# Performance work log

Measured on AMD Instinct MI355X. Metric: run time of the kernel, lower is better.

Reference implementation:

```python
import jax, jax.numpy as jnp
import numpy as np
from math import sqrt

DIM = 64
N_HEADS = 12
B, T = 4, 2048


def setup_inputs() -> dict:
    key = jax.random.key(0)
    ks = jax.random.split(key, 5)
    scale = 1.0 / sqrt(DIM)
    x = jax.random.normal(ks[0], (B, T, DIM), dtype=jnp.float32)
    # torch Linear(dim, h*dim) weight is (h*dim, dim); store transposed (dim, h*dim)
    Wq = jax.random.uniform(ks[1], (DIM, N_HEADS * DIM), dtype=jnp.float32, minval=-scale, maxval=scale)
    Wk = jax.random.uniform(ks[2], (DIM, N_HEADS * DIM), dtype=jnp.float32, minval=-scale, maxval=scale)
    Wv = jax.random.uniform(ks[3], (DIM, N_HEADS * DIM), dtype=jnp.float32, minval=-scale, maxval=scale)
    # finalDense: Linear(h*dim, dim) -> stored (h*dim, dim)
    Wo = jax.random.uniform(ks[4], (N_HEADS * DIM, DIM), dtype=jnp.float32,
                            minval=-1.0 / sqrt(N_HEADS * DIM), maxval=1.0 / sqrt(N_HEADS * DIM))
    return {"x": x, "Wq": Wq, "Wk": Wk, "Wv": Wv, "Wo": Wo}


def reference(x, Wq, Wk, Wv, Wo):
    b, t, k = x.shape
    h = Wq.shape[1] // k
    # NOTE: the original module does .view(b,t,h,k).view(b*h,t,k), a flat
    # row-major memory reinterpretation (NOT a head transpose). jnp.reshape
    # is the same flat reshape, so this is faithful.
    Q = (x @ Wq).reshape(b * h, t, k)
    K = (x @ Wk).reshape(b * h, t, k)
    V = (x @ Wv).reshape(b * h, t, k)
    # W[b,i,j] = sum_k K[b,i,k] * Q[b,j,k], scaled; softmax over j (last dim)
    W = jnp.einsum('bik,bjk->bij', K, Q) / sqrt(k)
    W = jax.nn.softmax(W, axis=2)
    Z = jnp.einsum('bij,bjk->bik', W, V)  # (b*h, t, k)
    Z = Z.reshape(b, t, h * k)  # flat reinterpretation, matches torch views
    return Z @ Wo
```

## Files before the change

kernel.cpp:

```cpp
#include <hip/hip_runtime.h>
#include <hip/hip_bf16.h>


#define DIM 64
#define NH 12
#define HD 768
#define BT 8192
#define TSEQ 2048
#define NSLICE 48
#define SLICE (TSEQ*DIM)

#define LDQ 72
#define LDP 72
#define LDT 72

typedef unsigned short ushort;
typedef __attribute__((ext_vector_type(8))) short bf16x8;
typedef __attribute__((ext_vector_type(4))) float f32x4;

#define SCALE2 0.18033688011112042f

__device__ __forceinline__ ushort f2b(float f) {
    union { float f; unsigned int i; } v; v.f = f;
    unsigned int x = v.i;
    return (ushort)((x + 0x7fffu + ((x >> 16) & 1u)) >> 16);
}

__global__ __launch_bounds__(256) void prep_w(
    const float* __restrict__ Wq, const float* __restrict__ Wk,
    const float* __restrict__ Wv, const float* __restrict__ Wo,
    ushort* __restrict__ Wt, ushort* __restrict__ Wot)
{
    __shared__ float tile[64][65];
    int bx = blockIdx.x;
    int z = bx / 12, bt = bx % 12;
    const float* __restrict__ IN = (z == 0) ? Wq : (z == 1) ? Wk : (z == 2) ? Wv : Wo;
    int inStride  = (z < 3) ? HD : DIM;
    int outStride = (z < 3) ? DIM : HD;
    int rbase = (z < 3) ? 0 : bt * 64;
    int cbase = (z < 3) ? bt * 64 : 0;
    ushort* __restrict__ OUT = (z < 3) ? (Wt + (size_t)z * HD * DIM) : Wot;
    int t = threadIdx.x;
    int r = t >> 2, c0 = (t & 3) * 16;
    #pragma unroll
    for (int cc = 0; cc < 16; cc += 4) {
        float4 a = *(const float4*)&IN[(size_t)(rbase + r) * inStride + cbase + c0 + cc];
        tile[r][c0 + cc] = a.x; tile[r][c0 + cc + 1] = a.y;
        tile[r][c0 + cc + 2] = a.z; tile[r][c0 + cc + 3] = a.w;
    }
    __syncthreads();
    int cl = t >> 2, r0 = (t & 3) * 16;
    ushort tmp[16] __attribute__((aligned(16)));
    #pragma unroll
    for (int rr = 0; rr < 16; ++rr) tmp[rr] = f2b(tile[r0 + rr][cl]);
    *(float4*)&OUT[(size_t)(cbase + cl) * outStride + rbase + r0] = *(const float4*)tmp;
    *(float4*)&OUT[(size_t)(cbase + cl) * outStride + rbase + r0 + 8] = *(const float4*)&tmp[8];
}

__global__ __launch_bounds__(256) void qkv_kernel(
    const float* __restrict__ x, const ushort* __restrict__ Wt,
    ushort* __restrict__ Q, ushort* __restrict__ K, ushort* __restrict__ V)
{
    int rt = blockIdx.x, half = blockIdx.y;
    int t = threadIdx.x, w = t >> 6, lane = t & 63;
    int ln = lane & 15, q = lane >> 4;
    int m0 = rt * 64 + w * 16;

    float4 xa = *(const float4*)&x[(size_t)(m0 + ln) * DIM + q * 8];
    float4 xb_ = *(const float4*)&x[(size_t)(m0 + ln) * DIM + q * 8 + 4];
    float4 xc = *(const float4*)&x[(size_t)(m0 + ln) * DIM + 32 + q * 8];
    float4 xd = *(const float4*)&x[(size_t)(m0 + ln) * DIM + 32 + q * 8 + 4];
    ushort ta[8] __attribute__((aligned(16)));
    ushort tb[8] __attribute__((aligned(16)));
    ta[0]=f2b(xa.x); ta[1]=f2b(xa.y); ta[2]=f2b(xa.z); ta[3]=f2b(xa.w);
    ta[4]=f2b(xb_.x); ta[5]=f2b(xb_.y); ta[6]=f2b(xb_.z); ta[7]=f2b(xb_.w);
    tb[0]=f2b(xc.x); tb[1]=f2b(xc.y); tb[2]=f2b(xc.z); tb[3]=f2b(xc.w);
    tb[4]=f2b(xd.x); tb[5]=f2b(xd.y); tb[6]=f2b(xd.z); tb[7]=f2b(xd.w);
    bf16x8 af0 = *(const bf16x8*)ta;
    bf16x8 af1 = *(const bf16x8*)tb;

    for (int cc = 0; cc < 18; ++cc) {
        int ct = half * 18 + cc;
        int which = ct / 12;
        int col0 = (ct % 12) * 64;
        const ushort* __restrict__ Wz = Wt + (size_t)which * HD * DIM;
        ushort* __restrict__ Y = (which == 0) ? Q : (which == 1) ? K : V;
        float sc = (which == 0) ? SCALE2 : 1.f;
        #pragma unroll
        for (int nt = 0; nt < 4; ++nt) {
            int n = col0 + nt * 16 + ln;
            bf16x8 bf0 = *(const bf16x8*)&Wz[(size_t)n * DIM + q * 8];
            bf16x8 bf1 = *(const bf16x8*)&Wz[(size_t)n * DIM + 32 + q * 8];
            f32x4 acc = (f32x4){0.f, 0.f, 0.f, 0.f};
            acc = __builtin_amdgcn_mfma_f32_16x16x32_bf16(af0, bf0, acc, 0, 0, 0);
            acc = __builtin_amdgcn_mfma_f32_16x16x32_bf16(af1, bf1, acc, 0, 0, 0);
            #pragma unroll
            for (int r = 0; r < 4; ++r)
                Y[(size_t)(m0 + q * 4 + r) * HD + col0 + nt * 16 + ln] = f2b(acc[r] * sc);
        }
    }
}

__global__ __launch_bounds__(256) void vtrans_kernel(
    const ushort* __restrict__ V, ushort* __restrict__ Vt)
{
    __shared__ ushort tileT[64 * LDT];
    int tt = blockIdx.x, s = blockIdx.y;
    const ushort* __restrict__ Vp = V + (size_t)s * SLICE;
    ushort* __restrict__ Vo = Vt + (size_t)s * SLICE;
    int t = threadIdx.x;
    int r = t >> 3, c = (t & 7) * 8;
    ushort va[8] __attribute__((aligned(16)));
    ushort vb[8] __attribute__((aligned(16)));
    *(float4*)va = *(const float4*)&Vp[(size_t)(tt * 64 + r) * DIM + c];
    *(float4*)vb = *(const float4*)&Vp[(size_t)(tt * 64 + r + 32) * DIM + c];
    int g0 = ((r >> 3) ^ (c >> 3)) * 8 + (r & 7);
    int g1 = (((r + 32) >> 3) ^ (c >> 3)) * 8 + (r & 7);
    #pragma unroll
    for (int k = 0; k < 8; ++k) {
        tileT[(c + k) * LDT + g0] = va[k];
        tileT[(c + k) * LDT + g1] = vb[k];
    }
    __syncthreads();
    #pragma unroll
    for (int j = 0; j < 2; ++j) {
        int flat = t + 256 * j;
        int d = flat >> 3, tg = flat & 7;
        int sg = tg ^ ((d >> 3) & 7);
        float4 vv = *(const float4*)&tileT[d * LDT + sg * 8];
        *(float4*)&Vo[(size_t)d * TSEQ + tt * 64 + tg * 8] = vv;
    }
}

__global__ __launch_bounds__(256) void attn_kernel(
    const ushort* __restrict__ Qs, const ushort* __restrict__ Ks,
    const ushort* __restrict__ Vts, ushort* __restrict__ Zs)
{
    __shared__ ushort Qt[64 * LDQ];
    __shared__ ushort Pw[128 * LDP];
    int itile = blockIdx.x, s = blockIdx.y;
    const ushort* __restrict__ Qp = Qs + (size_t)s * SLICE;
    const ushort* __restrict__ Kp = Ks + (size_t)s * SLICE;
    const ushort* __restrict__ Vp = Vts + (size_t)s * SLICE;
    ushort* __restrict__ Zp = Zs + (size_t)s * SLICE;
    int t = threadIdx.x, w = t >> 6, lane = t & 63;
    int ln = lane & 15, q = lane >> 4;

    bf16x8 kf[2][2];
    #pragma unroll
    for (int ih = 0; ih < 2; ++ih) {
        int i0 = itile * 128 + w * 32 + ih * 16 + ln;
        kf[ih][0] = *(const bf16x8*)&Kp[(size_t)i0 * DIM + q * 8];
        kf[ih][1] = *(const bf16x8*)&Kp[(size_t)i0 * DIM + 32 + q * 8];
    }
    f32x4 Of[2][4];
    #pragma unroll
    for (int ih = 0; ih < 2; ++ih)
        #pragma unroll
        for (int dt = 0; dt < 4; ++dt) Of[ih][dt] = (f32x4){0.f, 0.f, 0.f, 0.f};
    float lsum[2] = {0.f, 0.f};
    ushort* Pme = &Pw[w * 32 * LDP];

    int sr = t >> 3, sc = (t & 7) * 8;
    float4 qa0 = *(const float4*)&Qp[(size_t)sr * DIM + sc];
    float4 qa1 = *(const float4*)&Qp[(size_t)(sr + 32) * DIM + sc];

    for (int jt = 0; jt < TSEQ; jt += 64) {
        __syncthreads();
        *(float4*)&Qt[sr * LDQ + sc] = qa0;
        *(float4*)&Qt[(sr + 32) * LDQ + sc] = qa1;
        __syncthreads();
        if (jt + 64 < TSEQ) {
            qa0 = *(const float4*)&Qp[(size_t)(jt + 64 + sr) * DIM + sc];
            qa1 = *(const float4*)&Qp[(size_t)(jt + 64 + sr + 32) * DIM + sc];
        }
        bf16x8 vb[4][2];
        #pragma unroll
        for (int dt = 0; dt < 4; ++dt) {
            vb[dt][0] = *(const bf16x8*)&Vp[(size_t)(dt * 16 + ln) * TSEQ + jt + q * 8];
            vb[dt][1] = *(const bf16x8*)&Vp[(size_t)(dt * 16 + ln) * TSEQ + jt + 32 + q * 8];
        }

        f32x4 Sf[2][4];
        #pragma unroll
        for (int mt = 0; mt < 4; ++mt) {
            bf16x8 a0 = *(const bf16x8*)&Qt[(mt * 16 + ln) * LDQ + q * 8];
            bf16x8 a1 = *(const bf16x8*)&Qt[(mt * 16 + ln) * LDQ + 32 + q * 8];
            #pragma unroll
            for (int ih = 0; ih < 2; ++ih) {
                f32x4 acc = (f32x4){0.f, 0.f, 0.f, 0.f};
                acc = __builtin_amdgcn_mfma_f32_16x16x32_bf16(a0, kf[ih][0], acc, 0, 0, 0);
                acc = __builtin_amdgcn_mfma_f32_16x16x32_bf16(a1, kf[ih][1], acc, 0, 0, 0);
                Sf[ih][mt] = acc;
            }
        }
        #pragma unroll
        for (int ih = 0; ih < 2; ++ih) {
            float ls = 0.f;
            #pragma unroll
            for (int mt = 0; mt < 4; ++mt) {
                float p0 = __builtin_amdgcn_exp2f(Sf[ih][mt][0]);
                float p1 = __builtin_amdgcn_exp2f(Sf[ih][mt][1]);
                float p2 = __builtin_amdgcn_exp2f(Sf[ih][mt][2]);
                float p3 = __builtin_amdgcn_exp2f(Sf[ih][mt][3]);
                unsigned int b0 = __float_as_uint(p0), b1 = __float_as_uint(p1);
                unsigned int b2 = __float_as_uint(p2), b3 = __float_as_uint(p3);
                unsigned int t1 = b1 & 0xFFFF0000u, t3 = b3 & 0xFFFF0000u;
                unsigned int h01 = (b0 >> 16) | t1;
                unsigned int h23 = (b2 >> 16) | t3;
                ls += __uint_as_float(h01 << 16) + __uint_as_float(t1)
                    + __uint_as_float(h23 << 16) + __uint_as_float(t3);
                *(uint2*)&Pme[(ih * 16 + ln) * LDP + mt * 16 + q * 4] =
                    make_uint2(h01, h23);
            }
            lsum[ih] += ls;
        }
        bf16x8 pa[2][2];
        #pragma unroll
        for (int ih = 0; ih < 2; ++ih) {
            pa[ih][0] = *(const bf16x8*)&Pme[(ih * 16 + ln) * LDP + q * 8];
            pa[ih][1] = *(const bf16x8*)&Pme[(ih * 16 + ln) * LDP + 32 + q * 8];
        }
        #pragma unroll
        for (int dt = 0; dt < 4; ++dt)
            #pragma unroll
            for (int ih = 0; ih < 2; ++ih) {
                Of[ih][dt] = __builtin_amdgcn_mfma_f32_16x16x32_bf16(pa[ih][0], vb[dt][0], Of[ih][dt], 0, 0, 0);
                Of[ih][dt] = __builtin_amdgcn_mfma_f32_16x16x32_bf16(pa[ih][1], vb[dt][1], Of[ih][dt], 0, 0, 0);
            }
    }
    float linv_r[2][4];
    #pragma unroll
    for (int ih = 0; ih < 2; ++ih) {
        float l = lsum[ih];
        l += __shfl_xor(l, 16);
        l += __shfl_xor(l, 32);
        float linv = 1.f / l;
        #pragma unroll
        for (int r = 0; r < 4; ++r) linv_r[ih][r] = __shfl(linv, q * 4 + r);
    }
    #pragma unroll
    for (int ih = 0; ih < 2; ++ih)
        #pragma unroll
        for (int dt = 0; dt < 4; ++dt)
            #pragma unroll
            for (int r = 0; r < 4; ++r)
                Pme[(ih * 16 + q * 4 + r) * LDP + dt * 16 + ln] =
                    f2b(Of[ih][dt][r] * linv_r[ih][r]);
    __syncthreads();
    int zr = t >> 1, zc = (t & 1) * 32;
    size_t zoff = (size_t)(itile * 128 + zr) * DIM + zc;
    #pragma unroll
    for (int c4 = 0; c4 < 4; ++c4)
        *(float4*)&Zp[zoff + c4 * 8] = *(const float4*)&Pw[zr * LDP + zc + c4 * 8];
}

__global__ __launch_bounds__(64) void out_kernel(
    const ushort* __restrict__ Z, const ushort* __restrict__ Wot,
    float* __restrict__ out)
{
    int m0 = blockIdx.x * 16;
    int lane = threadIdx.x;
    int ln = lane & 15, q = lane >> 4;
    f32x4 acc[4];
    #pragma unroll
    for (int nt = 0; nt < 4; ++nt) acc[nt] = (f32x4){0.f, 0.f, 0.f, 0.f};
    for (int kc = 0; kc < 24; ++kc) {
        bf16x8 af = *(const bf16x8*)&Z[(size_t)(m0 + ln) * HD + kc * 32 + q * 8];
        #pragma unroll
        for (int nt = 0; nt < 4; ++nt) {
            bf16x8 bf = *(const bf16x8*)&Wot[(size_t)(nt * 16 + ln) * HD + kc * 32 + q * 8];
            acc[nt] = __builtin_amdgcn_mfma_f32_16x16x32_bf16(af, bf, acc[nt], 0, 0, 0);
        }
    }
    #pragma unroll
    for (int nt = 0; nt < 4; ++nt)
        #pragma unroll
        for (int r = 0; r < 4; ++r)
            out[(size_t)(m0 + q * 4 + r) * DIM + nt * 16 + ln] = acc[nt][r];
}

extern "C" void kernel_launch(void* const* d_in, const int* in_sizes, int n_in,
                              void* d_out, int out_size, void* d_ws, size_t ws_size,
                              hipStream_t stream)
{
    const float* x  = (const float*)d_in[0];
    const float* Wq = (const float*)d_in[1];
    const float* Wk = (const float*)d_in[2];
    const float* Wv = (const float*)d_in[3];
    const float* Wo = (const float*)d_in[4];
    float* out = (float*)d_out;

    const size_t n = (size_t)BT * HD;
    ushort* Q   = (ushort*)d_ws;
    ushort* K   = Q + n;
    ushort* V   = K + n;
    ushort* Vt  = V + n;
    ushort* Wt  = Vt;
    ushort* Wot = Vt + n;
    ushort* Z   = V;

    prep_w<<<48, 256, 0, stream>>>(Wq, Wk, Wv, Wo, Wt, Wot);
    qkv_kernel<<<dim3(128, 2), 256, 0, stream>>>(x, Wt, Q, K, V);
    vtrans_kernel<<<dim3(32, 48), 256, 0, stream>>>(V, Vt);
    attn_kernel<<<dim3(16, 48), 256, 0, stream>>>(Q, K, Vt, Z);
    out_kernel<<<512, 64, 0, stream>>>(Z, Wot, out);
}
```

Baseline: 208.8 us.

## Use two waves of 64 rows each and stage V tiles through LDS

The attention kernel now runs 128 threads per block instead of 256, and each wave handles 64 query rows instead of 32. This halves the number of waves that reload the shared Q/V tile and doubles the MFMA work per LDS fragment. V is prefetched into registers with coalesced loads and staged in a shared Vtile, replacing the per-wave strided global loads of V fragments. In exchange each wave holds more accumulator registers (Of and Sf double), which may lower occupancy, and each block has fewer waves to hide latency.

```diff
diff --git a/kernel.cpp b/kernel.cpp
--- a/kernel.cpp
+++ b/kernel.cpp
@@ -132,11 +132,12 @@
     }
 }
 
-__global__ __launch_bounds__(256) void attn_kernel(
+__global__ __launch_bounds__(128) void attn_kernel(
     const ushort* __restrict__ Qs, const ushort* __restrict__ Ks,
     const ushort* __restrict__ Vts, ushort* __restrict__ Zs)
 {
     __shared__ ushort Qt[64 * LDQ];
+    __shared__ ushort Vtile[64 * LDQ];
     __shared__ ushort Pw[128 * LDP];
     int itile = blockIdx.x, s = blockIdx.y;
     const ushort* __restrict__ Qp = Qs + (size_t)s * SLICE;
@@ -146,48 +147,52 @@
     int t = threadIdx.x, w = t >> 6, lane = t & 63;
     int ln = lane & 15, q = lane >> 4;
 
-    bf16x8 kf[2][2];
-    #pragma unroll
-    for (int ih = 0; ih < 2; ++ih) {
-        int i0 = itile * 128 + w * 32 + ih * 16 + ln;
+    bf16x8 kf[4][2];
+    #pragma unroll
+    for (int ih = 0; ih < 4; ++ih) {
+        int i0 = itile * 128 + w * 64 + ih * 16 + ln;
         kf[ih][0] = *(const bf16x8*)&Kp[(size_t)i0 * DIM + q * 8];
         kf[ih][1] = *(const bf16x8*)&Kp[(size_t)i0 * DIM + 32 + q * 8];
     }
-    f32x4 Of[2][4];
-    #pragma unroll
-    for (int ih = 0; ih < 2; ++ih)
+    f32x4 Of[4][4];
+    #pragma unroll
+    for (int ih = 0; ih < 4; ++ih)
         #pragma unroll
         for (int dt = 0; dt < 4; ++dt) Of[ih][dt] = (f32x4){0.f, 0.f, 0.f, 0.f};
-    float lsum[2] = {0.f, 0.f};
-    ushort* Pme = &Pw[w * 32 * LDP];
+    float lsum[4] = {0.f, 0.f, 0.f, 0.f};
+    ushort* Pme = &Pw[w * 64 * LDP];
 
     int sr = t >> 3, sc = (t & 7) * 8;
-    float4 qa0 = *(const float4*)&Qp[(size_t)sr * DIM + sc];
-    float4 qa1 = *(const float4*)&Qp[(size_t)(sr + 32) * DIM + sc];
+    float4 qa[4], va[4];
+    #pragma unroll
+    for (int k = 0; k < 4; ++k) {
+        qa[k] = *(const float4*)&Qp[(size_t)(sr + 16 * k) * DIM + sc];
+        va[k] = *(const float4*)&Vp[(size_t)(sr + 16 * k) * TSEQ + sc];
+    }
 
     for (int jt = 0; jt < TSEQ; jt += 64) {
         __syncthreads();
-        *(float4*)&Qt[sr * LDQ + sc] = qa0;
-        *(float4*)&Qt[(sr + 32) * LDQ + sc] = qa1;
+        #pragma unroll
+        for (int k = 0; k < 4; ++k) {
+            *(float4*)&Qt[(sr + 16 * k) * LDQ + sc] = qa[k];
+            *(float4*)&Vtile[(sr + 16 * k) * LDQ + sc] = va[k];
+        }
         __syncthreads();
         if (jt + 64 < TSEQ) {
-            qa0 = *(const float4*)&Qp[(size_t)(jt + 64 + sr) * DIM + sc];
-            qa1 = *(const float4*)&Qp[(size_t)(jt + 64 + sr + 32) * DIM + sc];
-        }
-        bf16x8 vb[4][2];
-        #pragma unroll
-        for (int dt = 0; dt < 4; ++dt) {
-            vb[dt][0] = *(const bf16x8*)&Vp[(size_t)(dt * 16 + ln) * TSEQ + jt + q * 8];
-            vb[dt][1] = *(const bf16x8*)&Vp[(size_t)(dt * 16 + ln) * TSEQ + jt + 32 + q * 8];
-        }
-
-        f32x4 Sf[2][4];
+            #pragma unroll
+            for (int k = 0; k < 4; ++k) {
+                qa[k] = *(const float4*)&Qp[(size_t)(jt + 64 + sr + 16 * k) * DIM + sc];
+                va[k] = *(const float4*)&Vp[(size_t)(sr + 16 * k) * TSEQ + jt + 64 + sc];
+            }
+        }
+
+        f32x4 Sf[4][4];
         #pragma unroll
         for (int mt = 0; mt < 4; ++mt) {
             bf16x8 a0 = *(const bf16x8*)&Qt[(mt * 16 + ln) * LDQ + q * 8];
             bf16x8 a1 = *(const bf16x8*)&Qt[(mt * 16 + ln) * LDQ + 32 + q * 8];
             #pragma unroll
-            for (int ih = 0; ih < 2; ++ih) {
+            for (int ih = 0; ih < 4; ++ih) {
                 f32x4 acc = (f32x4){0.f, 0.f, 0.f, 0.f};
                 acc = __builtin_amdgcn_mfma_f32_16x16x32_bf16(a0, kf[ih][0], acc, 0, 0, 0);
                 acc = __builtin_amdgcn_mfma_f32_16x16x32_bf16(a1, kf[ih][1], acc, 0, 0, 0);
@@ -195,7 +200,7 @@
             }
         }
         #pragma unroll
-        for (int ih = 0; ih < 2; ++ih) {
+        for (int ih = 0; ih < 4; ++ih) {
             float ls = 0.f;
             #pragma unroll
             for (int mt = 0; mt < 4; ++mt) {
@@ -215,23 +220,26 @@
             }
             lsum[ih] += ls;
         }
-        bf16x8 pa[2][2];
-        #pragma unroll
-        for (int ih = 0; ih < 2; ++ih) {
+        bf16x8 pa[4][2];
+        #pragma unroll
+        for (int ih = 0; ih < 4; ++ih) {
             pa[ih][0] = *(const bf16x8*)&Pme[(ih * 16 + ln) * LDP + q * 8];
             pa[ih][1] = *(const bf16x8*)&Pme[(ih * 16 + ln) * LDP + 32 + q * 8];
         }
         #pragma unroll
-        for (int dt = 0; dt < 4; ++dt)
-            #pragma unroll
-            for (int ih = 0; ih < 2; ++ih) {
-                Of[ih][dt] = __builtin_amdgcn_mfma_f32_16x16x32_bf16(pa[ih][0], vb[dt][0], Of[ih][dt], 0, 0, 0);
-                Of[ih][dt] = __builtin_amdgcn_mfma_f32_16x16x32_bf16(pa[ih][1], vb[dt][1], Of[ih][dt], 0, 0, 0);
+        for (int dt = 0; dt < 4; ++dt) {
+            bf16x8 vb0 = *(const bf16x8*)&Vtile[(dt * 16 + ln) * LDQ + q * 8];
+            bf16x8 vb1 = *(const bf16x8*)&Vtile[(dt * 16 + ln) * LDQ + 32 + q * 8];
+            #pragma unroll
+            for (int ih = 0; ih < 4; ++ih) {
+                Of[ih][dt] = __builtin_amdgcn_mfma_f32_16x16x32_bf16(pa[ih][0], vb0, Of[ih][dt], 0, 0, 0);
+                Of[ih][dt] = __builtin_amdgcn_mfma_f32_16x16x32_bf16(pa[ih][1], vb1, Of[ih][dt], 0, 0, 0);
             }
-    }
-    float linv_r[2][4];
-    #pragma unroll
-    for (int ih = 0; ih < 2; ++ih) {
+        }
+    }
+    float linv_r[4][4];
+    #pragma unroll
+    for (int ih = 0; ih < 4; ++ih) {
         float l = lsum[ih];
         l += __shfl_xor(l, 16);
         l += __shfl_xor(l, 32);
@@ -240,7 +248,7 @@
         for (int r = 0; r < 4; ++r) linv_r[ih][r] = __shfl(linv, q * 4 + r);
     }
     #pragma unroll
-    for (int ih = 0; ih < 2; ++ih)
+    for (int ih = 0; ih < 4; ++ih)
         #pragma unroll
         for (int dt = 0; dt < 4; ++dt)
             #pragma unroll
@@ -248,11 +256,12 @@
                 Pme[(ih * 16 + q * 4 + r) * LDP + dt * 16 + ln] =
                     f2b(Of[ih][dt][r] * linv_r[ih][r]);
     __syncthreads();
-    int zr = t >> 1, zc = (t & 1) * 32;
-    size_t zoff = (size_t)(itile * 128 + zr) * DIM + zc;
-    #pragma unroll
-    for (int c4 = 0; c4 < 4; ++c4)
-        *(float4*)&Zp[zoff + c4 * 8] = *(const float4*)&Pw[zr * LDP + zc + c4 * 8];
+    int zr = t;
+    const ushort* src = &Pw[(zr >> 6) * 64 * LDP + (zr & 63) * LDP];
+    size_t zoff = (size_t)(itile * 128 + zr) * DIM;
+    #pragma unroll
+    for (int c4 = 0; c4 < 8; ++c4)
+        *(float4*)&Zp[zoff + c4 * 8] = *(const float4*)&src[c4 * 8];
 }
 
 __global__ __launch_bounds__(64) void out_kernel(
@@ -303,6 +312,6 @@
     prep_w<<<48, 256, 0, stream>>>(Wq, Wk, Wv, Wo, Wt, Wot);
     qkv_kernel<<<dim3(128, 2), 256, 0, stream>>>(x, Wt, Q, K, V);
     vtrans_kernel<<<dim3(32, 48), 256, 0, stream>>>(V, Vt);
-    attn_kernel<<<dim3(16, 48), 256, 0, stream>>>(Q, K, Vt, Z);
+    attn_kernel<<<dim3(16, 48), 128, 0, stream>>>(Q, K, Vt, Z);
     out_kernel<<<512, 64, 0, stream>>>(Z, Wot, out);
 }
```

Measured after the change: 296.8 us. 42.1% more time.
